# Optimization experiments

Measured on AMD Instinct MI355X. Metric: run time of the kernel, lower is better.

## Reference

```python
import jax, jax.numpy as jnp
import numpy as np

N, H, L, OUT = 1048576, 128, 16, 2


def setup_inputs() -> dict:
    key = jax.random.key(0)
    k0, k1, k2, k3, k4 = jax.random.split(key, 5)
    s = 1.0 / np.sqrt(H)  # torch nn.Linear default init bound
    x = jax.random.normal(k0, (N, H), dtype=jnp.float32)
    W = jax.random.uniform(k1, (L, H, H), dtype=jnp.float32, minval=-s, maxval=s)
    b = jax.random.uniform(k2, (L, H), dtype=jnp.float32, minval=-s, maxval=s)
    Wout = jax.random.uniform(k3, (OUT, H), dtype=jnp.float32, minval=-s, maxval=s)
    bout = jax.random.uniform(k4, (OUT,), dtype=jnp.float32, minval=-s, maxval=s)
    return {"x": x, "W": W, "b": b, "Wout": Wout, "bout": bout}


def reference(x, W, b, Wout, bout):
    # layer weights; torch Linear convention: y = x @ W.T + b (W is [out,in]).
    def step(h, wb):
        w, bias = wb
        return jax.nn.relu(h @ w.T + bias), None

    h, _ = jax.lax.scan(step, x, (W, b))
    return h @ Wout.T + bout  # final Linear(128, 2)
```

## Files before the change

### kernel.cpp

```cpp
#include <hip/hip_runtime.h>


#define LAYERS 16
#define SLD    132

typedef __bf16 bf16x8 __attribute__((ext_vector_type(8)));
typedef float  f32x4  __attribute__((ext_vector_type(4)));

__device__ __forceinline__ unsigned short f2bf(float f) {
  unsigned u = __float_as_uint(f);
  u += 0x7fffu + ((u >> 16) & 1u);
  return (unsigned short)(u >> 16);
}

#if __has_builtin(__builtin_amdgcn_cvt_pk_bf16_f32)
typedef __bf16 bf16x2 __attribute__((ext_vector_type(2)));
__device__ __forceinline__ unsigned pkbf(float a, float b) {
  return __builtin_bit_cast(unsigned, __builtin_amdgcn_cvt_pk_bf16_f32(a, b));
}
#else
__device__ __forceinline__ unsigned pkbf(float a, float b) {
  return (((unsigned)f2bf(b)) << 16) | (unsigned)f2bf(a);
}
#endif

__device__ __forceinline__ void split2(float a, float b, unsigned &hw, unsigned &lw) {
  unsigned hp = pkbf(a, b);
  float la = a - __uint_as_float(hp << 16);
  float lb = b - __uint_as_float(hp & 0xffff0000u);
  hw = hp;
  lw = pkbf(la, lb);
}

__device__ __forceinline__ float upk(unsigned w) {
  return __uint_as_float(w & 0xffff0000u) + __uint_as_float(w << 16);
}

__global__ void prep_w(const float* __restrict__ W, unsigned* __restrict__ wf) {
  int t = blockIdx.x * 256 + threadIdx.x;
  int l     = t >> 14;
  int r     = t & 16383;
  int fi    = r >> 8;
  int inner = r & 255;
  int lanei = inner >> 2;
  int d     = inner & 3;
  int term  = fi & 1;
  int ntks  = fi >> 1;
  int nt = ntks >> 2, ks = ntks & 3;
  int n = nt * 16 + (lanei & 15);
  int k = ks * 32 + (lanei >> 4) * 8 + d * 2;
  const float* wp = W + ((l * 128 + n) * 128 + k);
  float w0 = wp[0], w1 = wp[1];
  unsigned hp = pkbf(w0, w1);
  unsigned res;
  if (term == 0) {
    res = hp;
  } else {
    float h0 = __uint_as_float(hp << 16);
    float h1 = __uint_as_float(hp & 0xffff0000u);
    res = pkbf(w0 - h0, w1 - h1);
  }
  wf[t] = res;
}

__launch_bounds__(256, 1)
__global__ void mlp_kernel(const unsigned* __restrict__ wf,
                           const float* __restrict__ bias,
                           const float* __restrict__ x,
                           const float* __restrict__ wout,
                           const float* __restrict__ bout,
                           float* __restrict__ out) {
  __shared__ unsigned sS[4 * 64 * SLD];
  const int tid  = threadIdx.x;
  const int wave = tid >> 6;
  const int lane = tid & 63;
  const int c    = lane & 15;
  const int q    = lane >> 4;
  const int s    = (c >> 2) & 3;
  const long rowbase = (long)blockIdx.x * 256 + wave * 64;

  unsigned* sw = sS + wave * (64 * SLD);

  uint4 a_hi[4][4];
  uint4 a_lo[4][4];

  {
    const float* xb = x + rowbase * 128;
#pragma unroll
    for (int mt = 0; mt < 4; ++mt) {
      const float* xr = xb + (mt * 16 + c) * 128 + q * 8;
#pragma unroll
      for (int ks = 0; ks < 4; ++ks) {
        float4 v0 = *(const float4*)(xr + ks * 32);
        float4 v1 = *(const float4*)(xr + ks * 32 + 4);
        uint4 hh, ll;
        split2(v0.x, v0.y, hh.x, ll.x);
        split2(v0.z, v0.w, hh.y, ll.y);
        split2(v1.x, v1.y, hh.z, ll.z);
        split2(v1.z, v1.w, hh.w, ll.w);
        a_hi[mt][ks] = hh;
        a_lo[mt][ks] = ll;
      }
    }
  }

#pragma unroll 1
  for (int l = 0; l < LAYERS; ++l) {
    if (l > 0) {
      __syncthreads();
#pragma unroll
      for (int mt = 0; mt < 4; ++mt) {
        const unsigned* rowp = sw + (mt * 16 + c) * SLD;
#pragma unroll
        for (int ks = 0; ks < 4; ++ks) {
          int fb = ks * 32 + 8 * (q ^ s);
          uint4 p0 = *(const uint4*)(rowp + fb);
          uint4 p1 = *(const uint4*)(rowp + fb + 4);
          uint4 hh, ll;
          hh.x = __builtin_amdgcn_perm(p0.y, p0.x, 0x07060302u);
          ll.x = __builtin_amdgcn_perm(p0.y, p0.x, 0x05040100u);
          hh.y = __builtin_amdgcn_perm(p0.w, p0.z, 0x07060302u);
          ll.y = __builtin_amdgcn_perm(p0.w, p0.z, 0x05040100u);
          hh.z = __builtin_amdgcn_perm(p1.y, p1.x, 0x07060302u);
          ll.z = __builtin_amdgcn_perm(p1.y, p1.x, 0x05040100u);
          hh.w = __builtin_amdgcn_perm(p1.w, p1.z, 0x07060302u);
          ll.w = __builtin_amdgcn_perm(p1.w, p1.z, 0x05040100u);
          a_hi[mt][ks] = hh;
          a_lo[mt][ks] = ll;
        }
      }
    }

    const uint4* wl = (const uint4*)(wf + l * 16384);
    float bv[8];
#pragma unroll
    for (int nt = 0; nt < 8; ++nt) bv[nt] = bias[l * 128 + nt * 16 + c];

#pragma unroll
    for (int nt = 0; nt < 8; ++nt) {
      uint4 bh[4], bl[4];
#pragma unroll
      for (int ks = 0; ks < 4; ++ks) {
        bh[ks] = wl[((nt * 4 + ks) * 2 + 0) * 64 + lane];
        bl[ks] = wl[((nt * 4 + ks) * 2 + 1) * 64 + lane];
      }
      f32x4 acc[4];
#pragma unroll
      for (int mt = 0; mt < 4; ++mt) {
        f32x4 a0 = {bv[nt], bv[nt], bv[nt], bv[nt]};
        acc[mt] = a0;
      }
#pragma unroll
      for (int ks = 0; ks < 4; ++ks) {
        bf16x8 Bh = __builtin_bit_cast(bf16x8, bh[ks]);
        bf16x8 Bl = __builtin_bit_cast(bf16x8, bl[ks]);
#pragma unroll
        for (int mt = 0; mt < 4; ++mt) {
          bf16x8 Ah = __builtin_bit_cast(bf16x8, a_hi[mt][ks]);
          bf16x8 Al = __builtin_bit_cast(bf16x8, a_lo[mt][ks]);
          acc[mt] = __builtin_amdgcn_mfma_f32_16x16x32_bf16(Ah, Bh, acc[mt], 0, 0, 0);
          acc[mt] = __builtin_amdgcn_mfma_f32_16x16x32_bf16(Ah, Bl, acc[mt], 0, 0, 0);
          acc[mt] = __builtin_amdgcn_mfma_f32_16x16x32_bf16(Al, Bh, acc[mt], 0, 0, 0);
        }
      }
#pragma unroll
      for (int mt = 0; mt < 4; ++mt) {
        int fsw = (nt * 16 + c) ^ (8 * q);
        unsigned* wp = sw + (mt * 16 + q * 4) * SLD + fsw;
        float e0 = fmaxf(acc[mt][0], 0.0f);
        float e1 = fmaxf(acc[mt][1], 0.0f);
        float e2 = fmaxf(acc[mt][2], 0.0f);
        float e3 = fmaxf(acc[mt][3], 0.0f);
        unsigned hp, lp, hp2, lp2;
        split2(e0, e1, hp, lp);
        split2(e2, e3, hp2, lp2);
        wp[0 * SLD] = (hp << 16) | (lp & 0xffffu);
        wp[1 * SLD] = (hp & 0xffff0000u) | (lp >> 16);
        wp[2 * SLD] = (hp2 << 16) | (lp2 & 0xffffu);
        wp[3 * SLD] = (hp2 & 0xffff0000u) | (lp2 >> 16);
      }
    }
  }

  __syncthreads();
  float bo0 = bout[0], bo1 = bout[1];
#pragma unroll
  for (int mt = 0; mt < 4; ++mt) {
    const unsigned* rowp = sw + (mt * 16 + c) * SLD;
    float s0 = 0.0f, s1 = 0.0f;
#pragma unroll
    for (int bb = 0; bb < 4; ++bb) {
      int fpb = q * 32 + bb * 8;
      int fab = q * 32 + (bb ^ s) * 8;
      uint4 h0 = *(const uint4*)(rowp + fpb);
      uint4 h1 = *(const uint4*)(rowp + fpb + 4);
      float4 w00 = *(const float4*)(wout + fab);
      float4 w01 = *(const float4*)(wout + fab + 4);
      float4 w10 = *(const float4*)(wout + 128 + fab);
      float4 w11 = *(const float4*)(wout + 128 + fab + 4);
      float xv;
      xv = upk(h0.x); s0 = fmaf(xv, w00.x, s0); s1 = fmaf(xv, w10.x, s1);
      xv = upk(h0.y); s0 = fmaf(xv, w00.y, s0); s1 = fmaf(xv, w10.y, s1);
      xv = upk(h0.z); s0 = fmaf(xv, w00.z, s0); s1 = fmaf(xv, w10.z, s1);
      xv = upk(h0.w); s0 = fmaf(xv, w00.w, s0); s1 = fmaf(xv, w10.w, s1);
      xv = upk(h1.x); s0 = fmaf(xv, w01.x, s0); s1 = fmaf(xv, w11.x, s1);
      xv = upk(h1.y); s0 = fmaf(xv, w01.y, s0); s1 = fmaf(xv, w11.y, s1);
      xv = upk(h1.z); s0 = fmaf(xv, w01.z, s0); s1 = fmaf(xv, w11.z, s1);
      xv = upk(h1.w); s0 = fmaf(xv, w01.w, s0); s1 = fmaf(xv, w11.w, s1);
    }
    s0 += __shfl_xor(s0, 16); s0 += __shfl_xor(s0, 32);
    s1 += __shfl_xor(s1, 16); s1 += __shfl_xor(s1, 32);
    if (q == 0) {
      long r = rowbase + mt * 16 + c;
      float2 o;
      o.x = s0 + bo0;
      o.y = s1 + bo1;
      *(float2*)(out + r * 2) = o;
    }
  }
}

extern "C" void kernel_launch(void* const* d_in, const int* in_sizes, int n_in,
                              void* d_out, int out_size, void* d_ws, size_t ws_size,
                              hipStream_t stream) {
  (void)in_sizes; (void)n_in; (void)out_size; (void)ws_size;
  const float* x    = (const float*)d_in[0];
  const float* W    = (const float*)d_in[1];
  const float* b    = (const float*)d_in[2];
  const float* wout = (const float*)d_in[3];
  const float* bout = (const float*)d_in[4];
  float* out = (float*)d_out;
  unsigned* wf = (unsigned*)d_ws;

  prep_w<<<dim3(1024), dim3(256), 0, stream>>>(W, wf);
  mlp_kernel<<<dim3(4096), dim3(256), 0, stream>>>(wf, b, x, wout, bout, out);
}
```

Measured before the change: 2.521 ms.

## Double-buffer weight fragment loads across tiles and layers, drop block barriers

Weight fragments are held in a two-slot register buffer. The loads for the next column tile, or the next layer's first tile, are issued before the current tile's MFMAs, so global/L2 latency overlaps compute. Next-layer bias values are also prefetched. The __syncthreads calls are removed because each wave only touches its own LDS region. In exchange the kernel uses more VGPRs and relies on the compiler keeping LDS ordering within a wave.

```diff
diff --git a/kernel.cpp b/kernel.cpp
--- a/kernel.cpp
+++ b/kernel.cpp
@@ -84,6 +84,19 @@
   uint4 a_hi[4][4];
   uint4 a_lo[4][4];
 
+  uint4 bhb[2][4], blb[2][4];
+  {
+    const uint4* wl0 = (const uint4*)wf;
+#pragma unroll
+    for (int ks = 0; ks < 4; ++ks) {
+      bhb[0][ks] = wl0[((0 * 4 + ks) * 2 + 0) * 64 + lane];
+      blb[0][ks] = wl0[((0 * 4 + ks) * 2 + 1) * 64 + lane];
+    }
+  }
+  float bv[8], bv_n[8];
+#pragma unroll
+  for (int nt = 0; nt < 8; ++nt) bv[nt] = bias[nt * 16 + c];
+
   {
     const float* xb = x + rowbase * 128;
 #pragma unroll
@@ -107,7 +120,6 @@
 #pragma unroll 1
   for (int l = 0; l < LAYERS; ++l) {
     if (l > 0) {
-      __syncthreads();
 #pragma unroll
       for (int mt = 0; mt < 4; ++mt) {
         const unsigned* rowp = sw + (mt * 16 + c) * SLD;
@@ -131,19 +143,33 @@
       }
     }
 
-    const uint4* wl = (const uint4*)(wf + l * 16384);
-    float bv[8];
-#pragma unroll
-    for (int nt = 0; nt < 8; ++nt) bv[nt] = bias[l * 128 + nt * 16 + c];
+    const uint4* wl      = (const uint4*)(wf + l * 16384);
+    const uint4* wl_next = (const uint4*)(wf + (l + 1) * 16384);
 
 #pragma unroll
     for (int nt = 0; nt < 8; ++nt) {
-      uint4 bh[4], bl[4];
-#pragma unroll
-      for (int ks = 0; ks < 4; ++ks) {
-        bh[ks] = wl[((nt * 4 + ks) * 2 + 0) * 64 + lane];
-        bl[ks] = wl[((nt * 4 + ks) * 2 + 1) * 64 + lane];
-      }
+      const uint4* bh = bhb[nt & 1];
+      const uint4* bl = blb[nt & 1];
+      uint4* bh_n = bhb[(nt + 1) & 1];
+      uint4* bl_n = blb[(nt + 1) & 1];
+      if (nt < 7) {
+#pragma unroll
+        for (int ks = 0; ks < 4; ++ks) {
+          bh_n[ks] = wl[(((nt + 1) * 4 + ks) * 2 + 0) * 64 + lane];
+          bl_n[ks] = wl[(((nt + 1) * 4 + ks) * 2 + 1) * 64 + lane];
+        }
+      } else if (l < LAYERS - 1) {
+#pragma unroll
+        for (int ks = 0; ks < 4; ++ks) {
+          bh_n[ks] = wl_next[((0 * 4 + ks) * 2 + 0) * 64 + lane];
+          bl_n[ks] = wl_next[((0 * 4 + ks) * 2 + 1) * 64 + lane];
+        }
+      }
+      if (nt == 0 && l < LAYERS - 1) {
+#pragma unroll
+        for (int j = 0; j < 8; ++j) bv_n[j] = bias[(l + 1) * 128 + j * 16 + c];
+      }
+
       f32x4 acc[4];
 #pragma unroll
       for (int mt = 0; mt < 4; ++mt) {
@@ -180,9 +206,10 @@
         wp[3 * SLD] = (hp2 & 0xffff0000u) | (lp2 >> 16);
       }
     }
-  }
-
-  __syncthreads();
+#pragma unroll
+    for (int j = 0; j < 8; ++j) bv[j] = bv_n[j];
+  }
+
   float bo0 = bout[0], bo1 = bout[1];
 #pragma unroll
   for (int mt = 0; mt < 4; ++mt) {
```

Result: faster. 2.178 ms (-13.6%).
